# Optimization experiments

Measured on AMD Instinct MI355X. Metric: run time of the kernel, lower is better.

## Reference

```python
import jax, jax.numpy as jnp
import numpy as np

B, S, H = 2, 2048, 4096
NH, NKV, HD = 32, 8, 128
GROUPS = NH // NKV
THETA = 10000.0


def _rope_cos_sin(position_ids):
    # inv_freq: [HD/2]
    inv_freq = 1.0 / (THETA ** (jnp.arange(0, HD, 2, dtype=jnp.float32) / HD))
    freqs = position_ids.astype(jnp.float32)[..., None] * inv_freq  # [B,S,HD/2]
    emb = jnp.concatenate([freqs, freqs], axis=-1)  # [B,S,HD]
    return jnp.cos(emb), jnp.sin(emb)


def _rotate_half(x):
    x1, x2 = jnp.split(x, 2, axis=-1)
    return jnp.concatenate([-x2, x1], axis=-1)


def setup_inputs() -> dict:
    key = jax.random.key(0)
    k1, k2, k3, k4, k5 = jax.random.split(key, 5)
    scale = 1.0 / np.sqrt(H)
    return {
        "hidden_states": jax.random.normal(k1, (B, S, H), dtype=jnp.float32),
        "position_ids": jnp.broadcast_to(jnp.arange(S, dtype=jnp.int64), (B, S)),
        "wq": jax.random.normal(k2, (NH * HD, H), dtype=jnp.float32) * scale,
        "wk": jax.random.normal(k3, (NKV * HD, H), dtype=jnp.float32) * scale,
        "wv": jax.random.normal(k4, (NKV * HD, H), dtype=jnp.float32) * scale,
        "wo": jax.random.normal(k5, (NH * HD, H), dtype=jnp.float32) * scale,
    }


def reference(hidden_states, position_ids, wq, wk, wv, wo):
    bsz, q_len, _ = hidden_states.shape
    # projections (nn.Linear: x @ W^T)
    q = jnp.einsum('bsh,dh->bsd', hidden_states, wq).reshape(bsz, q_len, NH, HD).transpose(0, 2, 1, 3)
    k = jnp.einsum('bsh,dh->bsd', hidden_states, wk).reshape(bsz, q_len, NKV, HD).transpose(0, 2, 1, 3)
    v = jnp.einsum('bsh,dh->bsd', hidden_states, wv).reshape(bsz, q_len, NKV, HD).transpose(0, 2, 1, 3)
    # RoPE
    cos, sin = _rope_cos_sin(position_ids)  # [B,S,HD]
    cos = cos[:, None, :, :]
    sin = sin[:, None, :, :]
    q = q * cos + _rotate_half(q) * sin
    k = k * cos + _rotate_half(k) * sin
    # repeat_kv (GQA expansion)
    k = jnp.repeat(k, GROUPS, axis=1)  # [B,NH,S,HD]
    v = jnp.repeat(v, GROUPS, axis=1)
    # scores + causal mask + softmax (fp32)
    scores = jnp.einsum('bhqd,bhkd->bhqk', q, k) / jnp.sqrt(jnp.float32(HD))
    causal = jnp.tril(jnp.ones((q_len, q_len), dtype=bool))
    scores = jnp.where(causal[None, None], scores, jnp.finfo(jnp.float32).min)
    attn = jax.nn.softmax(scores.astype(jnp.float32), axis=-1).astype(q.dtype)
    # AV + output projection
    out = jnp.einsum('bhqk,bhkd->bhqd', attn, v)
    out = out.transpose(0, 2, 1, 3).reshape(bsz, q_len, NH * HD)
    return jnp.einsum('bsd,hd->bsh', out, wo)
```

## Files before the change

kernel.cpp:

```cpp
#include <hip/hip_runtime.h>
#include <hip/hip_bf16.h>

#define B_    2
#define S_    2048
#define H_    4096
#define NH_   32
#define NKV_  8
#define HD_   128
#define M_    (B_*S_)
#define QKVN_ 6144

typedef unsigned short u16;
typedef __attribute__((ext_vector_type(8))) short bf16x8;
typedef __attribute__((ext_vector_type(4))) float f32x4;

__device__ __forceinline__ u16 f2bf(float x){
  unsigned u = __builtin_bit_cast(unsigned, x);
  unsigned r = u + 0x7fffu + ((u >> 16) & 1u);
  return (u16)(r >> 16);
}
__device__ __forceinline__ float bf2f(u16 x){
  unsigned u = ((unsigned)x) << 16;
  return __builtin_bit_cast(float, u);
}

__device__ __forceinline__ void gload_lds16(const u16* g, u16* l){
  __builtin_amdgcn_global_load_lds((const __attribute__((address_space(1))) void*)g,
                                   (__attribute__((address_space(3))) void*)l,
                                   16, 0, 0);
}

__global__ __launch_bounds__(256) void cast_bf16_k(const float* __restrict__ s,
                                                   u16* __restrict__ d, int n,
                                                   float sc){
  int i = (blockIdx.x * 256 + threadIdx.x) * 4;
  int stride = gridDim.x * 256 * 4;
  for (; i < n; i += stride){
    float4 v = *(const float4*)(s + i);
    uint2 o;
    o.x = (unsigned)f2bf(v.x * sc) | ((unsigned)f2bf(v.y * sc) << 16);
    o.y = (unsigned)f2bf(v.z * sc) | ((unsigned)f2bf(v.w * sc) << 16);
    *(uint2*)(d + i) = o;
  }
}

#define GBAR asm volatile("s_barrier" ::: "memory")
#define GLG0 asm volatile("s_waitcnt lgkmcnt(0)" ::: "memory")
#define GVM8 asm volatile("s_waitcnt vmcnt(8)" ::: "memory")

template<typename OutT>
__global__ __launch_bounds__(512, 2) void gemmr4_k(const u16* __restrict__ A,
                                                   const u16* __restrict__ Bw,
                                                   OutT* __restrict__ C,
                                                   int M, int N, int K){
  __shared__ u16 LDS[65536];
  u16* const Asl = LDS;
  u16* const Bsl = LDS + 32768;

  const int tid = threadIdx.x;
  const int wave = tid >> 6, lane = tid & 63;
  const int l15 = lane & 15, lhi = lane >> 4;
  const int wm = wave >> 2, wn = wave & 3;

  const int nwgx = gridDim.x;
  const int lin = blockIdx.y * nwgx + blockIdx.x;
  const int cpx = (nwgx * gridDim.y) >> 3;
  const int swz = (lin & 7) * cpx + (lin >> 3);
  const int m0 = (swz / nwgx) * 256;
  const int n0 = (swz % nwgx) * 256;

  const int NKT = K >> 5;
  const u16* Agl = A  + (size_t)m0 * K;
  const u16* Bgl = Bw + (size_t)n0 * K;

  const int rowInChunk = lane >> 2;
  const int srcColOff = (((lane & 3) ^ ((lane >> 3) & 3)) << 3);
  const int cA0 = wave * 2;

#define SA(t, j) gload_lds16(Agl + (size_t)((cA0 + (j)) * 16 + rowInChunk) * K + (t) * 32 + srcColOff, \
                             Asl + ((t) & 3) * 8192 + (cA0 + (j)) * 512)
#define SB(t, j) gload_lds16(Bgl + (size_t)((cA0 + (j)) * 16 + rowInChunk) * K + (t) * 32 + srcColOff, \
                             Bsl + ((t) & 3) * 8192 + (cA0 + (j)) * 512)

  const int rAb = wm * 128 + l15;
  const int rBb = wn * 64 + l15;
  const int aoff = rAb * 32 + ((lhi ^ ((rAb >> 1) & 3)) << 3);
  const int boff = rBb * 32 + ((lhi ^ ((rBb >> 1) & 3)) << 3);

  f32x4 acc[8][4] = {};

#pragma unroll
  for (int t = 0; t < 3; ++t){
    SA(t, 0); SA(t, 1); SB(t, 0); SB(t, 1);
  }
  GVM8;
  GBAR;

  for (int t = 0; t < NKT; ++t){
    const u16* as = Asl + (t & 3) * 8192;
    const u16* bs = Bsl + (t & 3) * 8192;
    int t3 = t + 3; if (t3 >= NKT) t3 -= NKT;

    bf16x8 aLo[4], aHi[4], bLo[2], bHi[2];

#pragma unroll
    for (int f = 0; f < 4; ++f) aLo[f] = *(const bf16x8*)(as + aoff + f * 512);
#pragma unroll
    for (int g = 0; g < 2; ++g) bLo[g] = *(const bf16x8*)(bs + boff + g * 512);
    SA(t3, 0);
    GBAR; GLG0;
    __builtin_amdgcn_s_setprio(1);
#pragma unroll
    for (int g = 0; g < 2; ++g)
#pragma unroll
      for (int f = 0; f < 4; ++f)
        acc[f][g] = __builtin_amdgcn_mfma_f32_16x16x32_bf16(aLo[f], bLo[g], acc[f][g], 0, 0, 0);
    __builtin_amdgcn_s_setprio(0);
    GBAR;

#pragma unroll
    for (int g = 0; g < 2; ++g) bHi[g] = *(const bf16x8*)(bs + boff + (2 + g) * 512);
    SA(t3, 1);
    GBAR; GLG0;
    __builtin_amdgcn_s_setprio(1);
#pragma unroll
    for (int g = 0; g < 2; ++g)
#pragma unroll
      for (int f = 0; f < 4; ++f)
        acc[f][2 + g] = __builtin_amdgcn_mfma_f32_16x16x32_bf16(aLo[f], bHi[g], acc[f][2 + g], 0, 0, 0);
    __builtin_amdgcn_s_setprio(0);
    GBAR;

#pragma unroll
    for (int f = 0; f < 4; ++f) aHi[f] = *(const bf16x8*)(as + aoff + (4 + f) * 512);
    SB(t3, 0);
    GBAR; GLG0;
    __builtin_amdgcn_s_setprio(1);
#pragma unroll
    for (int g = 0; g < 2; ++g)
#pragma unroll
      for (int f = 0; f < 4; ++f)
        acc[4 + f][g] = __builtin_amdgcn_mfma_f32_16x16x32_bf16(aHi[f], bLo[g], acc[4 + f][g], 0, 0, 0);
    __builtin_amdgcn_s_setprio(0);
    GBAR;

    SB(t3, 1);
    GBAR;
    __builtin_amdgcn_s_setprio(1);
#pragma unroll
    for (int g = 0; g < 2; ++g)
#pragma unroll
      for (int f = 0; f < 4; ++f)
        acc[4 + f][2 + g] = __builtin_amdgcn_mfma_f32_16x16x32_bf16(aHi[f], bHi[g], acc[4 + f][2 + g], 0, 0, 0);
    __builtin_amdgcn_s_setprio(0);
    GVM8;
    GBAR;
  }

#pragma unroll
  for (int f = 0; f < 8; ++f)
#pragma unroll
    for (int g = 0; g < 4; ++g)
#pragma unroll
      for (int r = 0; r < 4; ++r){
        int row = m0 + wm * 128 + f * 16 + lhi * 4 + r;
        int col = n0 + wn * 64 + g * 16 + l15;
        float v = acc[f][g][r];
        if constexpr (sizeof(OutT) == 2) C[(size_t)row * N + col] = (OutT)f2bf(v);
        else                             C[(size_t)row * N + col] = v;
      }
#undef SA
#undef SB
}

__global__ __launch_bounds__(256) void rope40_k(u16* __restrict__ X){
  int idx = blockIdx.x * 256 + threadIdx.x;
  int d   = idx & 63;
  int t2  = idx >> 6;
  int hh  = t2 % 40;
  int row = t2 / 40;
  int s   = row & (S_ - 1);
  float inv = __expf(-(float)d * 0.14391156932f);
  float ang = (float)s * inv;
  float sn = sinf(ang), cs = cosf(ang);
  size_t base = (size_t)row * QKVN_ + hh * 128;
  float x1 = bf2f(X[base + d]), x2 = bf2f(X[base + d + 64]);
  X[base + d]      = f2bf(x1 * cs - x2 * sn);
  X[base + d + 64] = f2bf(x2 * cs + x1 * sn);
}

__global__ __launch_bounds__(256) void vtrans_k(const u16* __restrict__ QKV,
                                                u16* __restrict__ Vt){
  __shared__ u16 t[32][33];
  int bkv = blockIdx.z;
  int b = bkv >> 3, kv = bkv & 7;
  int s0 = blockIdx.y * 32, d0 = blockIdx.x * 32;
  int tx = threadIdx.x, ty = threadIdx.y;
  const u16* src = QKV + (size_t)b * S_ * QKVN_ + 5120 + kv * HD_;
#pragma unroll
  for (int i = 0; i < 4; i++)
    t[ty + i*8][tx] = src[(size_t)(s0 + ty + i*8) * QKVN_ + d0 + tx];
  __syncthreads();
  u16* dst = Vt + (size_t)bkv * HD_ * S_;
#pragma unroll
  for (int i = 0; i < 4; i++)
    dst[(size_t)(d0 + ty + i*8) * S_ + s0 + tx] = t[tx][ty + i*8];
}

__global__ __launch_bounds__(256, 2) void attn_k(const u16* __restrict__ QKV,
                                                 const u16* __restrict__ Vt,
                                                 u16* __restrict__ O){
  __shared__ u16 SM[40960];
  u16* const Ks0 = SM;
  u16* const Ks1 = SM + 8192;
  u16* const Vs0 = SM + 16384;
  u16* const Vs1 = SM + 24576;

  const int lane = threadIdx.x & 63, wave = threadIdx.x >> 6;
  const int l15 = lane & 15, lhi = lane >> 4;
  u16* const Pw = SM + 32768 + wave * 2048;

  const int b = blockIdx.z, h = blockIdx.y;
  const int kvh = h >> 2;

  const u16* Kbase = QKV + (size_t)b * S_ * QKVN_ + 4096 + kvh * HD_;
  const u16* Vb    = Vt  + (size_t)(b * NKV_ + kvh) * HD_ * S_;

  const int krow_s = lane >> 4;
  const int kg     = lane & 15;
  const int vrow_s = lane >> 3;
  const int vcol_s = ((lane & 7) ^ vrow_s) * 8;
  const int swl    = (l15 & 7) << 3;

  bf16x8 ones;
#pragma unroll
  for (int i = 0; i < 8; i++) ones[i] = (short)0x3F80;

#define STAGE(tt, kd, vd) do {                                              \
    const int tkv_ = (tt) * 64;                                             \
    _Pragma("unroll")                                                       \
    for (int j_ = 0; j_ < 4; ++j_){                                         \
      const int i_ = wave * 4 + j_;                                         \
      const int kr_ = 4 * i_ + krow_s;                                      \
      const int kc_ = ((kg ^ (kr_ & 7)) << 3);                              \
      gload_lds16(Kbase + (size_t)(tkv_ + kr_) * QKVN_ + kc_, (kd) + i_ * 512); \
      const int vr_ = 8 * i_ + vrow_s;                                      \
      gload_lds16(Vb + (size_t)vr_ * S_ + tkv_ + vcol_s, (vd) + i_ * 512);  \
    }                                                                       \
  } while (0)

  for (int jj = 0; jj < 2; ++jj){
    const int J = (jj == 0) ? (int)blockIdx.x : (15 - (int)blockIdx.x);
    const int ntiles = 2 * J + 2;
    const int qg0 = J * 128 + wave * 32;

    bf16x8 aq0[4], aq1[4];
    const size_t qb0 = ((size_t)(b * S_) + qg0 + l15) * QKVN_ + h * HD_;
#pragma unroll
    for (int kb = 0; kb < 4; kb++){
      aq0[kb] = *(const bf16x8*)(QKV + qb0 + kb * 32 + lhi * 8);
      aq1[kb] = *(const bf16x8*)(QKV + qb0 + (size_t)16 * QKVN_ + kb * 32 + lhi * 8);
    }

    f32x4 o0[8] = {}, o1[8] = {};
    f32x4 os0 = {}, os1 = {};

    STAGE(0, Ks0, Vs0);
    __syncthreads();

    for (int t = 0; t < ntiles; ++t){
      const int sel = t & 1;
      const u16* ks = sel ? Ks1 : Ks0;
      const u16* vs = sel ? Vs1 : Vs0;
      if (t + 1 < ntiles){
        u16* kd = sel ? Ks0 : Ks1;
        u16* vd = sel ? Vs0 : Vs1;
        STAGE(t + 1, kd, vd);
      }
      const int kv0 = t * 64;

      f32x4 sa0[4] = {}, sa1[4] = {};
      __builtin_amdgcn_s_setprio(1);
#pragma unroll
      for (int n = 0; n < 4; n++){
        const u16* kr = ks + (n * 16 + l15) * 128;
#pragma unroll
        for (int kb = 0; kb < 4; kb++){
          bf16x8 bk = *(const bf16x8*)(kr + ((kb * 32 + lhi * 8) ^ swl));
          sa0[n] = __builtin_amdgcn_mfma_f32_16x16x32_bf16(aq0[kb], bk, sa0[n], 0, 0, 0);
          sa1[n] = __builtin_amdgcn_mfma_f32_16x16x32_bf16(aq1[kb], bk, sa1[n], 0, 0, 0);
        }
      }
      __builtin_amdgcn_s_setprio(0);

      const bool nm0 = (kv0 + 63) > qg0;
      const bool nm1 = (kv0 + 63) > qg0 + 16;
#pragma unroll
      for (int n = 0; n < 4; n++)
#pragma unroll
        for (int r = 0; r < 4; r++){
          const int col = kv0 + n * 16 + l15;
          const int prow = lhi * 4 + r;
          float v0 = sa0[n][r];
          if (nm0 && col > qg0 + prow) v0 = -1e30f;
          float v1 = sa1[n][r];
          if (nm1 && col > qg0 + 16 + prow) v1 = -1e30f;
          const int pc = (n * 16 + l15) ^ ((prow & 7) << 3);
          Pw[prow * 64 + pc]        = f2bf(__expf(v0));
          Pw[(16 + prow) * 64 + pc] = f2bf(__expf(v1));
        }
      asm volatile("s_waitcnt lgkmcnt(0)" ::: "memory");

      bf16x8 pa0[2], pa1[2];
#pragma unroll
      for (int kb2 = 0; kb2 < 2; kb2++){
        pa0[kb2] = *(const bf16x8*)(Pw + l15 * 64        + ((kb2 * 32 + lhi * 8) ^ swl));
        pa1[kb2] = *(const bf16x8*)(Pw + (16 + l15) * 64 + ((kb2 * 32 + lhi * 8) ^ swl));
      }

      __builtin_amdgcn_s_setprio(1);
#pragma unroll
      for (int f = 0; f < 8; f++){
        const u16* vr = vs + (f * 16 + l15) * 64;
#pragma unroll
        for (int kb2 = 0; kb2 < 2; kb2++){
          bf16x8 bv = *(const bf16x8*)(vr + ((kb2 * 32 + lhi * 8) ^ swl));
          o0[f] = __builtin_amdgcn_mfma_f32_16x16x32_bf16(pa0[kb2], bv, o0[f], 0, 0, 0);
          o1[f] = __builtin_amdgcn_mfma_f32_16x16x32_bf16(pa1[kb2], bv, o1[f], 0, 0, 0);
        }
      }
#pragma unroll
      for (int kb2 = 0; kb2 < 2; kb2++){
        os0 = __builtin_amdgcn_mfma_f32_16x16x32_bf16(pa0[kb2], ones, os0, 0, 0, 0);
        os1 = __builtin_amdgcn_mfma_f32_16x16x32_bf16(pa1[kb2], ones, os1, 0, 0, 0);
      }
      __builtin_amdgcn_s_setprio(0);
      __syncthreads();
    }

    float iv0[4], iv1[4];
#pragma unroll
    for (int r = 0; r < 4; r++){ iv0[r] = 1.0f / os0[r]; iv1[r] = 1.0f / os1[r]; }
#pragma unroll
    for (int f = 0; f < 8; f++)
#pragma unroll
      for (int r = 0; r < 4; r++){
        const size_t r0 = (size_t)(b * S_ + qg0 + lhi * 4 + r) * H_ + h * HD_ + f * 16 + l15;
        O[r0]                       = f2bf(o0[f][r] * iv0[r]);
        O[r0 + (size_t)16 * H_]     = f2bf(o1[f][r] * iv1[r]);
      }
  }
#undef STAGE
}

extern "C" void kernel_launch(void* const* d_in, const int* in_sizes, int n_in,
                              void* d_out, int out_size, void* d_ws, size_t ws_size,
                              hipStream_t stream) {
  const float* hs = (const float*)d_in[0];
  const float* wq = (const float*)d_in[2];
  const float* wk = (const float*)d_in[3];
  const float* wv = (const float*)d_in[4];
  const float* wo = (const float*)d_in[5];

  u16* wsp  = (u16*)d_ws;
  u16* hsb  = wsp;
  u16* wqkv = hsb + 16777216;
  u16* wob  = wqkv + 25165824;
  u16* QKV  = wob + 16777216;
  u16* Vt   = QKV + 25165824;
  u16* Oraw = Vt + 4194304;
  float* out = (float*)d_out;

  const float SCALE = 0.08838834764831845f;

  cast_bf16_k<<<2048, 256, 0, stream>>>(hs, hsb, M_ * H_, 1.0f);
  cast_bf16_k<<<2048, 256, 0, stream>>>(wq, wqkv, NH_ * HD_ * H_, SCALE);
  cast_bf16_k<<<2048, 256, 0, stream>>>(wk, wqkv + 16777216, NKV_ * HD_ * H_, 1.0f);
  cast_bf16_k<<<2048, 256, 0, stream>>>(wv, wqkv + 20971520, NKV_ * HD_ * H_, 1.0f);
  cast_bf16_k<<<2048, 256, 0, stream>>>(wo, wob, NH_ * HD_ * H_, 1.0f);

  gemmr4_k<u16><<<dim3(QKVN_ / 256, M_ / 256), 512, 0, stream>>>(hsb, wqkv, QKV, M_, QKVN_, H_);

  rope40_k<<<(B_ * S_ * 40 * 64) / 256, 256, 0, stream>>>(QKV);

  vtrans_k<<<dim3(HD_ / 32, S_ / 32, B_ * NKV_), dim3(32, 8), 0, stream>>>(QKV, Vt);

  attn_k<<<dim3(8, NH_, B_), 256, 0, stream>>>(QKV, Vt, Oraw);

  gemmr4_k<float><<<dim3(H_ / 256, M_ / 256), 512, 0, stream>>>(Oraw, wob, out, M_, H_, NH_ * HD_);
}
```

Measured before the change: 549.0 us.

## Fuse RoPE into QKV GEMM epilogue with permuted weights and double-buffered LDS

Permutes Q/K weight rows during the bf16 cast so that each RoPE pair (d, d+64) lands in accumulator tiles 16 columns apart inside one wave. RoPE can then be applied in the QKV GEMM epilogue using precomputed cos/sin tables, which removes the separate rope kernel and its read-modify-write pass over QKV. The GEMM also moves from a 4-stage to a 2-stage LDS ring (half the shared memory), which shortens the prefetch distance and adds sched_barriers. Risks include exposed load latency from the shallower pipeline and a layout dependency on the permutation that the attention kernel must tolerate.

```diff
diff --git a/kernel.cpp b/kernel.cpp
--- a/kernel.cpp
+++ b/kernel.cpp
@@ -9,6 +9,7 @@
 #define HD_   128
 #define M_    (B_*S_)
 #define QKVN_ 6144
+#define VOFF_ 5120
 
 typedef unsigned short u16;
 typedef __attribute__((ext_vector_type(8))) short bf16x8;
@@ -28,6 +29,16 @@
   __builtin_amdgcn_global_load_lds((const __attribute__((address_space(1))) void*)g,
                                    (__attribute__((address_space(3))) void*)l,
                                    16, 0, 0);
+}
+
+__global__ __launch_bounds__(256) void trig_k(float* __restrict__ ct,
+                                              float* __restrict__ st){
+  int i = blockIdx.x * 256 + threadIdx.x;
+  int s = i >> 6, dd = i & 63;
+  float inv = __expf(-(float)dd * 0.14391156932f);
+  float ang = (float)s * inv;
+  ct[i] = cosf(ang);
+  st[i] = sinf(ang);
 }
 
 __global__ __launch_bounds__(256) void cast_bf16_k(const float* __restrict__ s,
@@ -44,18 +55,39 @@
   }
 }
 
+__global__ __launch_bounds__(256) void cast_perm_k(const float* __restrict__ s,
+                                                   u16* __restrict__ d, int n,
+                                                   float sc){
+  int i = (blockIdx.x * 256 + threadIdx.x) * 4;
+  int stride = gridDim.x * 256 * 4;
+  for (; i < n; i += stride){
+    const int row = i >> 12, col = i & 4095;
+    const int dd = row & 127;
+    const int perm = ((dd & 63) >> 4) * 32 + ((dd >> 6) << 4) + (dd & 15);
+    const size_t o = (size_t)((row & ~127) | perm) * 4096 + col;
+    float4 v = *(const float4*)(s + i);
+    uint2 w;
+    w.x = (unsigned)f2bf(v.x * sc) | ((unsigned)f2bf(v.y * sc) << 16);
+    w.y = (unsigned)f2bf(v.z * sc) | ((unsigned)f2bf(v.w * sc) << 16);
+    *(uint2*)(d + o) = w;
+  }
+}
+
 #define GBAR asm volatile("s_barrier" ::: "memory")
 #define GLG0 asm volatile("s_waitcnt lgkmcnt(0)" ::: "memory")
-#define GVM8 asm volatile("s_waitcnt vmcnt(8)" ::: "memory")
+#define GVM1 asm volatile("s_waitcnt vmcnt(1)" ::: "memory")
+#define GSB0 __builtin_amdgcn_sched_barrier(0)
 
 template<typename OutT>
-__global__ __launch_bounds__(512, 2) void gemmr4_k(const u16* __restrict__ A,
+__global__ __launch_bounds__(512, 2) void gemmd2_k(const u16* __restrict__ A,
                                                    const u16* __restrict__ Bw,
                                                    OutT* __restrict__ C,
+                                                   const float* __restrict__ Ct,
+                                                   const float* __restrict__ St,
                                                    int M, int N, int K){
-  __shared__ u16 LDS[65536];
+  __shared__ u16 LDS[32768];
   u16* const Asl = LDS;
-  u16* const Bsl = LDS + 32768;
+  u16* const Bsl = LDS + 16384;
 
   const int tid = threadIdx.x;
   const int wave = tid >> 6, lane = tid & 63;
@@ -78,9 +110,9 @@
   const int cA0 = wave * 2;
 
 #define SA(t, j) gload_lds16(Agl + (size_t)((cA0 + (j)) * 16 + rowInChunk) * K + (t) * 32 + srcColOff, \
-                             Asl + ((t) & 3) * 8192 + (cA0 + (j)) * 512)
+                             Asl + ((t) & 1) * 8192 + (cA0 + (j)) * 512)
 #define SB(t, j) gload_lds16(Bgl + (size_t)((cA0 + (j)) * 16 + rowInChunk) * K + (t) * 32 + srcColOff, \
-                             Bsl + ((t) & 3) * 8192 + (cA0 + (j)) * 512)
+                             Bsl + ((t) & 1) * 8192 + (cA0 + (j)) * 512)
 
   const int rAb = wm * 128 + l15;
   const int rBb = wn * 64 + l15;
@@ -89,17 +121,16 @@
 
   f32x4 acc[8][4] = {};
 
-#pragma unroll
-  for (int t = 0; t < 3; ++t){
-    SA(t, 0); SA(t, 1); SB(t, 0); SB(t, 1);
-  }
-  GVM8;
+  SA(0, 0); SA(0, 1); SB(0, 0); SB(0, 1);
+  SA(1, 0);
+  GVM1;
   GBAR;
 
   for (int t = 0; t < NKT; ++t){
-    const u16* as = Asl + (t & 3) * 8192;
-    const u16* bs = Bsl + (t & 3) * 8192;
-    int t3 = t + 3; if (t3 >= NKT) t3 -= NKT;
+    const u16* as = Asl + (t & 1) * 8192;
+    const u16* bs = Bsl + (t & 1) * 8192;
+    int t1 = t + 1; if (t1 >= NKT) t1 -= NKT;
+    int t2 = t + 2; if (t2 >= NKT) t2 -= NKT;
 
     bf16x8 aLo[4], aHi[4], bLo[2], bHi[2];
 
@@ -107,8 +138,8 @@
     for (int f = 0; f < 4; ++f) aLo[f] = *(const bf16x8*)(as + aoff + f * 512);
 #pragma unroll
     for (int g = 0; g < 2; ++g) bLo[g] = *(const bf16x8*)(bs + boff + g * 512);
-    SA(t3, 0);
-    GBAR; GLG0;
+    SA(t1, 1);
+    GBAR; GLG0; GSB0;
     __builtin_amdgcn_s_setprio(1);
 #pragma unroll
     for (int g = 0; g < 2; ++g)
@@ -116,12 +147,12 @@
       for (int f = 0; f < 4; ++f)
         acc[f][g] = __builtin_amdgcn_mfma_f32_16x16x32_bf16(aLo[f], bLo[g], acc[f][g], 0, 0, 0);
     __builtin_amdgcn_s_setprio(0);
-    GBAR;
+    GSB0; GBAR;
 
 #pragma unroll
     for (int g = 0; g < 2; ++g) bHi[g] = *(const bf16x8*)(bs + boff + (2 + g) * 512);
-    SA(t3, 1);
-    GBAR; GLG0;
+    SB(t1, 0);
+    GBAR; GLG0; GSB0;
     __builtin_amdgcn_s_setprio(1);
 #pragma unroll
     for (int g = 0; g < 2; ++g)
@@ -129,12 +160,12 @@
       for (int f = 0; f < 4; ++f)
         acc[f][2 + g] = __builtin_amdgcn_mfma_f32_16x16x32_bf16(aLo[f], bHi[g], acc[f][2 + g], 0, 0, 0);
     __builtin_amdgcn_s_setprio(0);
-    GBAR;
+    GSB0; GBAR;
 
 #pragma unroll
     for (int f = 0; f < 4; ++f) aHi[f] = *(const bf16x8*)(as + aoff + (4 + f) * 512);
-    SB(t3, 0);
-    GBAR; GLG0;
+    SB(t1, 1);
+    GBAR; GLG0; GSB0;
     __builtin_amdgcn_s_setprio(1);
 #pragma unroll
     for (int g = 0; g < 2; ++g)
@@ -142,9 +173,9 @@
       for (int f = 0; f < 4; ++f)
         acc[4 + f][g] = __builtin_amdgcn_mfma_f32_16x16x32_bf16(aHi[f], bLo[g], acc[4 + f][g], 0, 0, 0);
     __builtin_amdgcn_s_setprio(0);
-    GBAR;
-
-    SB(t3, 1);
+    GSB0; GBAR;
+
+    SA(t2, 0);
     GBAR;
     __builtin_amdgcn_s_setprio(1);
 #pragma unroll
@@ -153,40 +184,43 @@
       for (int f = 0; f < 4; ++f)
         acc[4 + f][2 + g] = __builtin_amdgcn_mfma_f32_16x16x32_bf16(aHi[f], bHi[g], acc[4 + f][2 + g], 0, 0, 0);
     __builtin_amdgcn_s_setprio(0);
-    GVM8;
-    GBAR;
+    GSB0; GVM1; GBAR;
   }
 
-#pragma unroll
-  for (int f = 0; f < 8; ++f)
-#pragma unroll
-    for (int g = 0; g < 4; ++g)
-#pragma unroll
-      for (int r = 0; r < 4; ++r){
-        int row = m0 + wm * 128 + f * 16 + lhi * 4 + r;
-        int col = n0 + wn * 64 + g * 16 + l15;
-        float v = acc[f][g][r];
-        if constexpr (sizeof(OutT) == 2) C[(size_t)row * N + col] = (OutT)f2bf(v);
-        else                             C[(size_t)row * N + col] = v;
-      }
+  if constexpr (sizeof(OutT) == 2){
+    const bool qk = (n0 < VOFF_);
+#pragma unroll
+    for (int f = 0; f < 8; ++f)
+#pragma unroll
+      for (int gp = 0; gp < 2; ++gp){
+        const int g = gp * 2;
+        const int dd = ((wn & 1) * 2 + gp) * 16 + l15;
+        const size_t c0 = (size_t)(n0 + wn * 64 + g * 16 + l15);
+#pragma unroll
+        for (int r = 0; r < 4; ++r){
+          const int row = m0 + wm * 128 + f * 16 + lhi * 4 + r;
+          const int sidx = ((row & (S_ - 1)) << 6) + dd;
+          float cs = 1.0f, sn = 0.0f;
+          if (qk){ cs = Ct[sidx]; sn = St[sidx]; }
+          const float x1 = acc[f][g][r], x2 = acc[f][g + 1][r];
+          C[(size_t)row * N + c0]      = (OutT)f2bf(x1 * cs - x2 * sn);
+          C[(size_t)row * N + c0 + 16] = (OutT)f2bf(x2 * cs + x1 * sn);
+        }
+      }
+  } else {
+#pragma unroll
+    for (int f = 0; f < 8; ++f)
+#pragma unroll
+      for (int g = 0; g < 4; ++g)
+#pragma unroll
+        for (int r = 0; r < 4; ++r){
+          int row = m0 + wm * 128 + f * 16 + lhi * 4 + r;
+          int col = n0 + wn * 64 + g * 16 + l15;
+          C[(size_t)row * N + col] = acc[f][g][r];
+        }
+  }
 #undef SA
 #undef SB
-}
-
-__global__ __launch_bounds__(256) void rope40_k(u16* __restrict__ X){
-  int idx = blockIdx.x * 256 + threadIdx.x;
-  int d   = idx & 63;
-  int t2  = idx >> 6;
-  int hh  = t2 % 40;
-  int row = t2 / 40;
-  int s   = row & (S_ - 1);
-  float inv = __expf(-(float)d * 0.14391156932f);
-  float ang = (float)s * inv;
-  float sn = sinf(ang), cs = cosf(ang);
-  size_t base = (size_t)row * QKVN_ + hh * 128;
-  float x1 = bf2f(X[base + d]), x2 = bf2f(X[base + d + 64]);
-  X[base + d]      = f2bf(x1 * cs - x2 * sn);
-  X[base + d + 64] = f2bf(x2 * cs + x1 * sn);
 }
 
 __global__ __launch_bounds__(256) void vtrans_k(const u16* __restrict__ QKV,
@@ -196,7 +230,7 @@
   int b = bkv >> 3, kv = bkv & 7;
   int s0 = blockIdx.y * 32, d0 = blockIdx.x * 32;
   int tx = threadIdx.x, ty = threadIdx.y;
-  const u16* src = QKV + (size_t)b * S_ * QKVN_ + 5120 + kv * HD_;
+  const u16* src = QKV + (size_t)b * S_ * QKVN_ + VOFF_ + kv * HD_;
 #pragma unroll
   for (int i = 0; i < 4; i++)
     t[ty + i*8][tx] = src[(size_t)(s0 + ty + i*8) * QKVN_ + d0 + tx];
@@ -369,23 +403,25 @@
   u16* QKV  = wob + 16777216;
   u16* Vt   = QKV + 25165824;
   u16* Oraw = Vt + 4194304;
+  float* Ct = (float*)(Oraw + 16777216);
+  float* St = Ct + 131072;
   float* out = (float*)d_out;
 
   const float SCALE = 0.08838834764831845f;
 
+  trig_k<<<512, 256, 0, stream>>>(Ct, St);
+
   cast_bf16_k<<<2048, 256, 0, stream>>>(hs, hsb, M_ * H_, 1.0f);
-  cast_bf16_k<<<2048, 256, 0, stream>>>(wq, wqkv, NH_ * HD_ * H_, SCALE);
-  cast_bf16_k<<<2048, 256, 0, stream>>>(wk, wqkv + 16777216, NKV_ * HD_ * H_, 1.0f);
+  cast_perm_k<<<2048, 256, 0, stream>>>(wq, wqkv, NH_ * HD_ * H_, SCALE);
+  cast_perm_k<<<2048, 256, 0, stream>>>(wk, wqkv + 16777216, NKV_ * HD_ * H_, 1.0f);
   cast_bf16_k<<<2048, 256, 0, stream>>>(wv, wqkv + 20971520, NKV_ * HD_ * H_, 1.0f);
   cast_bf16_k<<<2048, 256, 0, stream>>>(wo, wob, NH_ * HD_ * H_, 1.0f);
 
-  gemmr4_k<u16><<<dim3(QKVN_ / 256, M_ / 256), 512, 0, stream>>>(hsb, wqkv, QKV, M_, QKVN_, H_);
-
-  rope40_k<<<(B_ * S_ * 40 * 64) / 256, 256, 0, stream>>>(QKV);
+  gemmd2_k<u16><<<dim3(QKVN_ / 256, M_ / 256), 512, 0, stream>>>(hsb, wqkv, QKV, Ct, St, M_, QKVN_, H_);
 
   vtrans_k<<<dim3(HD_ / 32, S_ / 32, B_ * NKV_), dim3(32, 8), 0, stream>>>(QKV, Vt);
 
   attn_k<<<dim3(8, NH_, B_), 256, 0, stream>>>(QKV, Vt, Oraw);
 
-  gemmr4_k<float><<<dim3(H_ / 256, M_ / 256), 512, 0, stream>>>(Oraw, wob, out, M_, H_, NH_ * HD_);
-}
+  gemmd2_k<float><<<dim3(H_ / 256, M_ / 256), 512, 0, stream>>>(Oraw, wob, out, nullptr, nullptr, M_, H_, NH_ * HD_);
+}
```

After: 571.7 us. +4.1%, slower.
